# Performance work log

Hardware: AMD Instinct MI355X
Metric: run time of the kernel (lower is better)

## Reference

```python
import jax, jax.numpy as jnp
import numpy as np

D = 128           # volume / particle box size (pixels)
B = 8             # particles per batch
K = 125           # SO(3) grid poses (5x5x5 around each center Euler)
TOPK = 2          # keep_top_k_values
MAX_SHIFT_FRAC = 0.25  # main_config.projmatching.max_shift_fraction


def setup_inputs() -> dict:
    key = jax.random.key(0)
    k1, k2, k3, k4 = jax.random.split(key, 4)
    vol = jax.random.normal(k1, (D, D, D), dtype=jnp.float32)
    parts = jax.random.normal(k2, (B, D, D), dtype=jnp.float32)
    ctf = jax.random.uniform(k3, (B, D, D // 2 + 1), dtype=jnp.float32)
    euler_degs = jax.random.normal(k4, (K, 3), dtype=jnp.float32) * 8.0
    return {"vol": vol, "parts": parts, "ctf": ctf, "euler_degs": euler_degs}


def _rot_z(t):
    c, s = jnp.cos(t), jnp.sin(t)
    z, o = jnp.zeros_like(t), jnp.ones_like(t)
    return jnp.stack([jnp.stack([c, -s, z], -1),
                      jnp.stack([s, c, z], -1),
                      jnp.stack([z, z, o], -1)], -2)


def _rot_y(t):
    c, s = jnp.cos(t), jnp.sin(t)
    z, o = jnp.zeros_like(t), jnp.ones_like(t)
    return jnp.stack([jnp.stack([c, z, s], -1),
                      jnp.stack([z, o, z], -1),
                      jnp.stack([-s, z, c], -1)], -2)


def euler_zyz_to_matrix(degs):
    # RELION Euler convention ZYZ: R = Rz(a) @ Ry(b) @ Rz(c)
    rad = jnp.deg2rad(degs)
    return _rot_z(rad[..., 0]) @ _rot_y(rad[..., 1]) @ _rot_z(rad[..., 2])


def trilinear_sample(vol, zi, yi, xi):
    # vol: (Dz, Dy, W) complex64; coords: (K, h, w) float32 array indices
    Dz, Dy, W = vol.shape
    z0, y0, x0 = jnp.floor(zi), jnp.floor(yi), jnp.floor(xi)
    tz, ty, tx = zi - z0, yi - y0, xi - x0
    out = jnp.zeros(zi.shape, dtype=vol.dtype)
    for dz in (0, 1):
        wz = tz if dz else 1.0 - tz
        zc = z0 + dz
        vz = (zc >= 0) & (zc < Dz)
        zdx = jnp.clip(zc, 0, Dz - 1).astype(jnp.int32)
        for dy in (0, 1):
            wy = ty if dy else 1.0 - ty
            yc = y0 + dy
            vy = (yc >= 0) & (yc < Dy)
            ydx = jnp.clip(yc, 0, Dy - 1).astype(jnp.int32)
            for dx in (0, 1):
                wx = tx if dx else 1.0 - tx
                xc = x0 + dx
                vx = (xc >= 0) & (xc < W)
                xdx = jnp.clip(xc, 0, W - 1).astype(jnp.int32)
                w = jnp.where(vz & vy & vx, wz * wy * wx, 0.0)
                out = out + w * vol[zdx, ydx, xdx]
    return out


def project_fourier(vol_rfft, rotmats):
    # extract_central_slices_rfft: pose-dependent gather+trilinear interp of a
    # central slice from the fftshifted 3D rfft volume. Output: (K, D, D//2+1).
    d = D
    w = d // 2 + 1
    y = jnp.arange(d, dtype=jnp.float32) - d // 2   # fftshifted full-dim freqs (pixel units)
    x = jnp.arange(w, dtype=jnp.float32)            # rfft (non-negative) freqs
    yy, xx = jnp.meshgrid(y, x, indexing='ij')      # (d, w)
    coords = jnp.stack([xx, yy, jnp.zeros_like(yy)], -1)       # xyz, (d, w, 3), z = 0 plane
    rot = jnp.einsum('kij,hwj->khwi', rotmats, coords)          # (K, d, w, 3) rotated xyz
    conj_mask = rot[..., 0] < 0                                  # Hermitian symmetry: flip to x>=0 half
    rot = jnp.where(conj_mask[..., None], -rot, rot)
    xi = rot[..., 0]
    yi = rot[..., 1] + d // 2
    zi = rot[..., 2] + d // 2
    samples = trilinear_sample(vol_rfft, zi, yi, xi)
    samples = jnp.where(conj_mask, jnp.conj(samples), samples)
    r2 = xx ** 2 + yy ** 2                                       # zero beyond Nyquist radius
    samples = jnp.where(r2[None] > (d // 2) ** 2, 0.0, samples)
    return samples


def reference(vol, parts, ctf, euler_degs):
    # compute_dft: rfft volume, fftshift non-rfft dims
    vol_rfft = jnp.fft.fftshift(jnp.fft.rfftn(vol), axes=(0, 1))
    parts_rfft = jnp.fft.fftshift(jnp.fft.rfft2(parts), axes=(-2,))  # (B, D, W)
    rotmats = euler_zyz_to_matrix(euler_degs)                        # (K, 3, 3)
    projs = project_fourier(vol_rfft, rotmats)                       # (K, D, W)
    projs = ctf[:, None] * projs[None]                               # _apply_ctfF: (B, K, D, W)
    # correlate_dft_2d: cross-correlation via iFFT of parts * conj(projs)
    prod = parts_rfft[:, None] * jnp.conj(projs)
    prod = jnp.fft.ifftshift(prod, axes=(-2,))
    corr = jnp.fft.irfft2(prod, s=(D, D))                            # (B, K, D, D)
    corr = jnp.fft.fftshift(corr, axes=(-2, -1))                     # zero shift at center
    # _extract_ccor_max: restrict to |shift| <= max_shift_fraction*D, take top-k peaks
    center = D // 2
    max_shift = int(MAX_SHIFT_FRAC * D)
    idx = jnp.arange(D) - center
    win = (jnp.abs(idx)[:, None] <= max_shift) & (jnp.abs(idx)[None, :] <= max_shift)
    masked = jnp.where(win, corr, -jnp.inf)
    flat = masked.reshape(B, K, D * D)
    vals, top_idx = jax.lax.top_k(flat, TOPK)                        # (B, K, TOPK)
    shifts = jnp.stack([top_idx // D - center, top_idx % D - center], -1)  # (B, K, TOPK, 2) yx
    return vals, shifts
```

## Files before the change

### kernel.cpp

```cpp
#include <hip/hip_runtime.h>
#include <math.h>

#define D 128
#define W 65
#define NK 125
#define NB 8
#define SLAB (D*W)
#define TWO_PI 6.28318530717958647692f
#define R2C 0.70710678118654752440f
#define C8C 0.92387953251128675613f
#define S8C 0.38268343236508977173f


__device__ __forceinline__ bool better(float va, int ia, float vb, int ib) {
    return (va > vb) || (va == vb && ia < ib);
}
__device__ __forceinline__ float2 cmul(float2 a, float2 b) {
    return make_float2(a.x*b.x - a.y*b.y, a.x*b.y + a.y*b.x);
}
__device__ __forceinline__ void cmac(float2& acc, float2 a, float2 b) {
    acc.x = fmaf(a.x, b.x, fmaf(-a.y, b.y, acc.x));
    acc.y = fmaf(a.x, b.y, fmaf( a.y, b.x, acc.y));
}
__device__ __forceinline__ float2 cadd(float2 a, float2 b){ return make_float2(a.x+b.x, a.y+b.y); }
__device__ __forceinline__ float2 csub(float2 a, float2 b){ return make_float2(a.x-b.x, a.y-b.y); }

__device__ __forceinline__ void fft8_fwd(const float2* x, float2* a) {
    float2 e0 = x[0], o0 = x[1], e1 = x[2], o1 = x[3];
    float2 e2 = x[4], o2 = x[5], e3 = x[6], o3 = x[7];
    float2 t0 = cadd(e0, e2), t1 = csub(e0, e2);
    float2 t2 = cadd(e1, e3), t3 = csub(e1, e3);
    float2 E0 = cadd(t0, t2), E2 = csub(t0, t2);
    float2 E1 = make_float2(t1.x + t3.y, t1.y - t3.x);
    float2 E3 = make_float2(t1.x - t3.y, t1.y + t3.x);
    float2 u0 = cadd(o0, o2), u1 = csub(o0, o2);
    float2 u2 = cadd(o1, o3), u3 = csub(o1, o3);
    float2 O0 = cadd(u0, u2), O2 = csub(u0, u2);
    float2 O1 = make_float2(u1.x + u3.y, u1.y - u3.x);
    float2 O3 = make_float2(u1.x - u3.y, u1.y + u3.x);
    float2 w1 = make_float2(R2C*(O1.x + O1.y), R2C*(O1.y - O1.x));
    float2 w2 = make_float2(O2.y, -O2.x);
    float2 w3 = make_float2(R2C*(O3.y - O3.x), -R2C*(O3.x + O3.y));
    a[0] = cadd(E0, O0); a[4] = csub(E0, O0);
    a[1] = cadd(E1, w1); a[5] = csub(E1, w1);
    a[2] = cadd(E2, w2); a[6] = csub(E2, w2);
    a[3] = cadd(E3, w3); a[7] = csub(E3, w3);
}

__device__ __forceinline__ void ifft8_store(float2* __restrict__ Ab, const float2* p,
                                            int l, int m0) {
    float2 e0 = p[0], o0 = p[1], e1 = p[2], o1 = p[3];
    float2 e2 = p[4], o2 = p[5], e3 = p[6], o3 = p[7];
    float2 t0 = cadd(e0, e2), t1 = csub(e0, e2);
    float2 t2 = cadd(e1, e3), t3 = csub(e1, e3);
    float2 E0 = cadd(t0, t2), E2 = csub(t0, t2);
    float2 E1 = make_float2(t1.x - t3.y, t1.y + t3.x);
    float2 E3 = make_float2(t1.x + t3.y, t1.y - t3.x);
    float2 u0 = cadd(o0, o2), u1 = csub(o0, o2);
    float2 u2 = cadd(o1, o3), u3 = csub(o1, o3);
    float2 O0 = cadd(u0, u2), O2 = csub(u0, u2);
    float2 O1 = make_float2(u1.x - u3.y, u1.y + u3.x);
    float2 O3 = make_float2(u1.x + u3.y, u1.y - u3.x);
    float2 w1o = make_float2(R2C*(O1.x - O1.y), R2C*(O1.x + O1.y));
    float2 w2o = make_float2(-O2.y, O2.x);
    float2 w3o = make_float2(R2C*(-O3.x - O3.y), R2C*(O3.x - O3.y));
    float2* A = Ab + l * 144 + m0;
    A[0*18] = cadd(E0, O0);
    A[4*18] = csub(E0, O0);
    A[1*18] = cadd(E1, w1o);
    A[5*18] = csub(E1, w1o);
    A[2*18] = cadd(E2, w2o);
    A[6*18] = csub(E2, w2o);
    A[3*18] = cadd(E3, w3o);
    A[7*18] = csub(E3, w3o);
}


template<int MODE>
__device__ __forceinline__ void fft128v2(const float* __restrict__ inf,
                                         const float2* __restrict__ inc,
                                         float2* __restrict__ out,
                                         int l0, int nlines,
                                         float2* __restrict__ Fl,
                                         float2* __restrict__ twf) {
    int tid = threadIdx.x;
    int line, t;
    if (MODE == 0) { t = tid & 7; line = tid >> 3; }
    else           { line = tid & 31; t = tid >> 5; }
    int l = l0 + line;
    bool live = (l < nlines);

    if (tid < 128) {
        float s, c;
        sincosf(-TWO_PI * (float)tid / 128.0f, &s, &c);
        twf[tid] = make_float2(c, s);
    }

    int base = 0, stride = 1;
    if (MODE == 1 || MODE == 3) { base = (l / W) * SLAB + (l % W); stride = W; }
    else if (MODE == 2) { base = l; stride = SLAB; }

    float2 xe[8], xo[8];
    if (live) {
        if (MODE == 0) {
            const float* r = inf + (size_t)l * D;
            #pragma unroll
            for (int j = 0; j < 8; ++j) {
                xe[j] = make_float2(r[t + 16*j], 0.f);
                xo[j] = make_float2(r[t + 8 + 16*j], 0.f);
            }
        } else {
            #pragma unroll
            for (int j = 0; j < 8; ++j) {
                xe[j] = inc[base + (t + 16*j) * stride];
                xo[j] = inc[base + (t + 8 + 16*j) * stride];
            }
        }
    } else {
        #pragma unroll
        for (int j = 0; j < 8; ++j) { xe[j] = make_float2(0,0); xo[j] = make_float2(0,0); }
    }
    float2 E[8], O[8];
    fft8_fwd(xe, E);
    fft8_fwd(xo, O);
    {
        const float2 w16[8] = {
            { 1.f, 0.f }, { C8C, -S8C }, { R2C, -R2C }, { S8C, -C8C },
            { 0.f, -1.f }, { -S8C, -C8C }, { -R2C, -R2C }, { -C8C, -S8C }
        };
        float2* Fp = Fl + line * 137 + t * 17;
        #pragma unroll
        for (int kk = 0; kk < 8; ++kk) {
            float2 wo = cmul(w16[kk], O[kk]);
            Fp[kk]     = cadd(E[kk], wo);
            Fp[kk + 8] = csub(E[kk], wo);
        }
    }
    __syncthreads();
    if (live) {
        const float2* Fr = Fl + line * 137;
        #pragma unroll
        for (int s = 0; s < 16; ++s) {
            int slot = t + 8 * s;
            if (MODE == 0 && slot > 64) break;
            int k = (MODE == 0) ? slot : (slot ^ 64);
            int kk = k & 15;
            float2 acc = make_float2(0.f, 0.f);
            #pragma unroll
            for (int tt = 0; tt < 8; ++tt) {
                cmac(acc, Fr[tt * 17 + kk], twf[(tt * k) & 127]);
            }
            if (MODE == 0)      out[(size_t)l * W + slot] = acc;
            else if (MODE == 3) out[(size_t)l * D + slot] = acc;
            else                out[base + slot * stride] = acc;
        }
    }
}


__global__ __launch_bounds__(256) void k1_kernel(const float* __restrict__ vol,
                                                 const float* __restrict__ parts,
                                                 const float* __restrict__ ctf,
                                                 const float* __restrict__ euler,
                                                 float2* __restrict__ bufA,
                                                 float2* __restrict__ pT1,
                                                 float* __restrict__ CT,
                                                 float* __restrict__ rot) {
    __shared__ float2 Fl[32 * 137];
    __shared__ float2 twf[128];
    int bid = blockIdx.x;
    int tid = threadIdx.x;
    if (bid < 512) {
        fft128v2<0>(vol, nullptr, bufA, bid * 32, D*D, Fl, twf);
    } else if (bid < 544) {
        fft128v2<0>(parts, nullptr, pT1, (bid - 512) * 32, NB*D, Fl, twf);
    } else if (bid == 544) {
        int k = tid;
        if (k < NK) {
            const float d2r = 0.017453292519943295f;
            float a = euler[k*3+0]*d2r, b = euler[k*3+1]*d2r, c = euler[k*3+2]*d2r;
            float sa, ca, sb, cb, sc, cc;
            sincosf(a, &sa, &ca); sincosf(b, &sb, &cb); sincosf(c, &sc, &cc);
            rot[k*9+0] =  ca*cb*cc - sa*sc;
            rot[k*9+1] = -ca*cb*sc - sa*cc;
            rot[k*9+2] =  ca*sb;
            rot[k*9+3] =  sa*cb*cc + ca*sc;
            rot[k*9+4] = -sa*cb*sc + ca*cc;
            rot[k*9+5] =  sa*sb;
            rot[k*9+6] = -sb*cc;
            rot[k*9+7] =  sb*sc;
            rot[k*9+8] =  cb;
        }
    } else {
        int i = (bid - 545) * 256 + tid;
        if (i < NB * W * D) {
            int m = i & (D-1);
            int t2 = i >> 7;
            int x = t2 % W;
            int b = t2 / W;
            CT[i] = ctf[b * SLAB + m * W + x];
        }
    }
}

__global__ __launch_bounds__(256) void k2_kernel(const float2* __restrict__ bufA,
                                                 float2* __restrict__ bufB,
                                                 const float2* __restrict__ pT1,
                                                 float2* __restrict__ QT) {
    __shared__ float2 Fl[32 * 137];
    __shared__ float2 twf[128];
    int bid = blockIdx.x;
    if (bid < 260) fft128v2<1>(nullptr, bufA, bufB, bid * 32, D*W, Fl, twf);
    else           fft128v2<3>(nullptr, pT1, QT, (bid - 260) * 32, NB*W, Fl, twf);
}

__global__ __launch_bounds__(256) void k3_kernel(const float2* __restrict__ bufB,
                                                 float2* __restrict__ bufA) {
    __shared__ float2 Fl[32 * 137];
    __shared__ float2 twf[128];
    fft128v2<2>(nullptr, bufB, bufA, blockIdx.x * 32, SLAB, Fl, twf);
}


__global__ void proj_kernel(const float2* __restrict__ vol, const float* __restrict__ rot,
                            float2* __restrict__ projT) {
    int idx = blockIdx.x * blockDim.x + threadIdx.x;
    if (idx >= NK * D * W) return;
    int h = idx & (D-1);
    int t2 = idx >> 7;
    int w = t2 % W;
    int k = t2 / W;
    float x = (float)w;
    float y = (float)(h - 64);
    const float* R = rot + k*9;
    float rx = R[0]*x + R[1]*y;
    float ry = R[3]*x + R[4]*y;
    float rz = R[6]*x + R[7]*y;
    bool neg = rx < 0.0f;
    if (neg) { rx = -rx; ry = -ry; rz = -rz; }
    float xi = rx;
    float yi = ry + 64.0f;
    float zi = rz + 64.0f;
    float z0 = floorf(zi), y0 = floorf(yi), x0 = floorf(xi);
    float tz = zi - z0, ty = yi - y0, tx = xi - x0;
    int z0i = (int)z0, y0i = (int)y0, x0i = (int)x0;
    float ar = 0.f, ai = 0.f;
    for (int dz = 0; dz < 2; ++dz) {
        float wz = dz ? tz : 1.0f - tz;
        int zc = z0i + dz;
        bool vz = (zc >= 0) && (zc < D);
        int zx = min(max(zc, 0), D-1);
        for (int dy = 0; dy < 2; ++dy) {
            float wy = dy ? ty : 1.0f - ty;
            int yc = y0i + dy;
            bool vy = (yc >= 0) && (yc < D);
            int yx = min(max(yc, 0), D-1);
            for (int dx = 0; dx < 2; ++dx) {
                float wx = dx ? tx : 1.0f - tx;
                int xc = x0i + dx;
                bool vx = (xc >= 0) && (xc < W);
                int xx = min(max(xc, 0), W-1);
                float wt = (vz && vy && vx) ? wz*wy*wx : 0.0f;
                float2 v = vol[zx * SLAB + yx * W + xx];
                ar = fmaf(wt, v.x, ar);
                ai = fmaf(wt, v.y, ai);
            }
        }
    }
    if (neg) ai = -ai;
    int yy = h - 64;
    if (w*w + yy*yy > 4096) { ar = 0.f; ai = 0.f; }
    projT[idx] = make_float2(ar, ai);
}


__global__ __launch_bounds__(256, 2) void corr_kernel(const float2* __restrict__ QT,
                                                      const float*  __restrict__ CT,
                                                      const float2* __restrict__ PJT,
                                                      float* __restrict__ outv) {
    __shared__ float2 tw[128];
    __shared__ float2 Ab[17*144];
    __shared__ float2 BC[32*67];
    __shared__ float  Ny[65];
    __shared__ float  redv[8];
    __shared__ int    redi[8];

    int g = blockIdx.x;
    int logical = (g & 7) * 125 + (g >> 3);
    int k = logical >> 3;
    int b = logical & 7;
    int tid = threadIdx.x;
    const float inv_d = 1.0f / 128.0f;

    if (tid < 128) {
        float s, c;
        sincosf(TWO_PI * (float)tid / 128.0f, &s, &c);
        tw[tid] = make_float2(c, s);
    }

    const float2* Qb = QT + b * (W * D);
    const float*  Cb = CT + b * (W * D);
    const float2* Jk = PJT + k * (W * D);

    int lane = tid & 63;
    int wv = tid >> 6;
    int sv = lane & 7;
    int vp = (96 + lane) & 127;
    float acc[16];
    #pragma unroll
    for (int j = 0; j < 16; ++j) acc[j] = 0.0f;
    float accR = 0.0f;
    int ur = 0, vr = 0;
    if (tid < 129) { if (tid < 65) { ur = 64; vr = tid; } else { ur = tid - 65; vr = 64; } }

    __syncthreads();

    float2 wvp = tw[vp];
    float2 tq = make_float2(1.0f, 0.0f);

    int l1 = tid >> 4, m01 = tid & 15;
    float2 Qv[8]; float Cv[8]; float2 Jv[8];

    for (int cg = 0; cg < 4; ++cg) {
        if (cg == 0) {
            for (int i = tid; i < 17 * 16; i += 256) {
                int l = i >> 4, m0 = i & 15;
                int x = (l < 16) ? ((l >> 2) + 16 * (l & 3)) : 64;
                const float2* Qx = Qb + x * 128 + m0;
                const float*  Cx = Cb + x * 128 + m0;
                const float2* Jx = Jk + x * 128 + m0;
                float2 p[8];
                #pragma unroll
                for (int j = 0; j < 8; ++j) {
                    float2 qv = Qx[16*j];
                    float  cf = Cx[16*j];
                    float2 pj = Jx[16*j];
                    float sx = qv.x * cf, sy = qv.y * cf;
                    p[j] = make_float2(sx*pj.x + sy*pj.y, sy*pj.x - sx*pj.y);
                }
                ifft8_store(Ab, p, l, m0);
            }
        } else {
            float2 p[8];
            #pragma unroll
            for (int j = 0; j < 8; ++j) {
                float sx = Qv[j].x * Cv[j], sy = Qv[j].y * Cv[j];
                p[j] = make_float2(sx*Jv[j].x + sy*Jv[j].y, sy*Jv[j].x - sx*Jv[j].y);
            }
            ifft8_store(Ab, p, l1, m01);
        }
        __syncthreads();
        if (cg < 3) {
            int xn = 4*(cg+1) + (l1 >> 2) + 16 * (l1 & 3);
            const float2* Qx = Qb + xn * 128 + m01;
            const float*  Cx = Cb + xn * 128 + m01;
            const float2* Jx = Jk + xn * 128 + m01;
            #pragma unroll
            for (int j = 0; j < 8; ++j) {
                Qv[j] = Qx[16*j];
                Cv[j] = Cx[16*j];
                Jv[j] = Jx[16*j];
            }
        }
        {
            int lim = (cg == 0) ? 325 : 260;
            for (int i = tid; i < lim; i += 256) {
                if (i < 260) {
                    int q = i / 65;
                    int u2 = i - q * 65;
                    int r = u2 & 7, up = (96 + u2) & 127;
                    float2 wup = tw[up];
                    float2 wup2 = cmul(wup, wup);
                    const float4* A0 = (const float4*)(Ab + (4*q+0)*144 + r*18);
                    const float4* A1 = (const float4*)(Ab + (4*q+1)*144 + r*18);
                    const float4* A2 = (const float4*)(Ab + (4*q+2)*144 + r*18);
                    const float4* A3 = (const float4*)(Ab + (4*q+3)*144 + r*18);
                    float2 g0{0,0}, g1{0,0}, g2{0,0}, g3{0,0};
                    float2 tA = make_float2(1.0f, 0.0f);
                    #pragma unroll
                    for (int h = 0; h < 8; ++h) {
                        float2 tB = cmul(tA, wup);
                        float4 a;
                        a = A0[h]; cmac(g0, make_float2(a.x,a.y), tA); cmac(g0, make_float2(a.z,a.w), tB);
                        a = A1[h]; cmac(g1, make_float2(a.x,a.y), tA); cmac(g1, make_float2(a.z,a.w), tB);
                        a = A2[h]; cmac(g2, make_float2(a.x,a.y), tA); cmac(g2, make_float2(a.z,a.w), tB);
                        a = A3[h]; cmac(g3, make_float2(a.x,a.y), tA); cmac(g3, make_float2(a.z,a.w), tB);
                        tA = cmul(tA, wup2);
                    }
                    float sg = (u2 & 1) ? -inv_d : inv_d;
                    g0.x *= sg; g0.y *= sg; g1.x *= sg; g1.y *= sg;
                    g2.x *= sg; g2.y *= sg; g3.x *= sg; g3.y *= sg;
                    if (cg == 0 && q == 0) { g0.x *= 0.5f; g0.y *= 0.5f; }
                    float2 h0 = g0, h1 = g1, h2 = g2, h3 = g3;
                    const float sc = 2.0f * inv_d;
                    float2 p1 = make_float2(R2C*(h1.x - h1.y), R2C*(h1.x + h1.y));
                    float2 q1 = make_float2(R2C*(-h1.x - h1.y), R2C*(h1.x - h1.y));
                    float2 i1 = make_float2(-h1.y, h1.x);
                    float2 i2 = make_float2(-h2.y, h2.x);
                    float2 n2 = make_float2( h2.y, -h2.x);
                    float2 p3 = make_float2(R2C*(h3.x - h3.y), R2C*(h3.x + h3.y));
                    float2 q3 = make_float2(R2C*(-h3.x - h3.y), R2C*(h3.x - h3.y));
                    float2 i3 = make_float2(-h3.y, h3.x);
                    float2 a02 = cadd(h0, h2), s02 = csub(h0, h2);
                    float2 s0 = cadd(a02, cadd(h1, h3));
                    float2 s4 = csub(a02, cadd(h1, h3));
                    float2 s2 = cadd(s02, csub(i1, i3));
                    float2 s6 = csub(s02, csub(i1, i3));
                    float2 b0i = cadd(h0, i2);
                    float2 b0n = cadd(h0, n2);
                    float2 s1 = cadd(b0i, cadd(p1, q3));
                    float2 s5 = csub(b0i, cadd(p1, q3));
                    float2 s3 = cadd(b0n, cadd(q1, p3));
                    float2 s7 = csub(b0n, cadd(q1, p3));
                    float2* Bp = BC + q * (8*67) + u2;
                    Bp[0*67] = make_float2(s0.x*sc, s0.y*sc);
                    Bp[1*67] = make_float2(s1.x*sc, s1.y*sc);
                    Bp[2*67] = make_float2(s2.x*sc, s2.y*sc);
                    Bp[3*67] = make_float2(s3.x*sc, s3.y*sc);
                    Bp[4*67] = make_float2(s4.x*sc, s4.y*sc);
                    Bp[5*67] = make_float2(s5.x*sc, s5.y*sc);
                    Bp[6*67] = make_float2(s6.x*sc, s6.y*sc);
                    Bp[7*67] = make_float2(s7.x*sc, s7.y*sc);
                } else {
                    int u2 = i - 260;
                    int r = u2 & 7, up = (96 + u2) & 127;
                    float2 wup = tw[up];
                    float2 wup2 = cmul(wup, wup);
                    const float4* A = (const float4*)(Ab + 16*144 + r*18);
                    float re = 0.0f;
                    float2 tA = make_float2(1.0f, 0.0f);
                    #pragma unroll
                    for (int h = 0; h < 8; ++h) {
                        float2 tB = cmul(tA, wup);
                        float4 a = A[h];
                        re = fmaf(a.x, tA.x, fmaf(-a.y, tA.y, re));
                        re = fmaf(a.z, tB.x, fmaf(-a.w, tB.y, re));
                        tA = cmul(tA, wup2);
                    }
                    Ny[u2] = ((u2 & 1) ? -inv_d : inv_d) * re;
                }
            }
        }
        __syncthreads();
        {
            #pragma unroll
            for (int q = 0; q < 4; ++q) {
                const float2* Bq = BC + (q * 8 + sv) * 67 + wv * 16;
                float tx = tq.x, ty = tq.y;
                #pragma unroll
                for (int j = 0; j < 16; ++j) {
                    float2 bv = Bq[j];
                    acc[j] = fmaf(bv.x, tx, fmaf(-bv.y, ty, acc[j]));
                }
                tq = cmul(tq, wvp);
            }
            if (cg == 0) {
                float sgn = (lane & 1) ? -inv_d : inv_d;
                #pragma unroll
                for (int j = 0; j < 16; ++j) acc[j] = fmaf(sgn, Ny[wv * 16 + j], acc[j]);
            }
            if (tid < 129) {
                int sr = vr & 7, vpr = (96 + vr) & 127;
                float a = accR;
                #pragma unroll
                for (int q = 0; q < 4; ++q) {
                    float2 t = tw[((4*cg + q) * vpr) & 127];
                    float2 bv = BC[(q * 8 + sr) * 67 + ur];
                    a = fmaf(bv.x, t.x, fmaf(-bv.y, t.y, a));
                }
                if (cg == 0) a += (vr & 1) ? -inv_d * Ny[ur] : inv_d * Ny[ur];
                accR = a;
            }
        }
        __syncthreads();
    }

    float v1 = -INFINITY, v2 = -INFINITY;
    int i1 = 0x7fffffff, i2 = 0x7fffffff;
    #pragma unroll
    for (int j = 0; j < 16; ++j) {
        float val = acc[j];
        int uu = wv * 16 + j;
        int fl = (32 + uu) * D + (32 + lane);
        if (better(val, fl, v1, i1)) { v2 = v1; i2 = i1; v1 = val; i1 = fl; }
        else if (better(val, fl, v2, i2)) { v2 = val; i2 = fl; }
    }
    if (tid < 129) {
        int fl = (32 + ur) * D + (32 + vr);
        if (better(accR, fl, v1, i1)) { v2 = v1; i2 = i1; v1 = accR; i1 = fl; }
        else if (better(accR, fl, v2, i2)) { v2 = accR; i2 = fl; }
    }
    for (int off = 32; off > 0; off >>= 1) {
        float b1 = __shfl_down(v1, off); int j1 = __shfl_down(i1, off);
        float b2 = __shfl_down(v2, off); int j2 = __shfl_down(i2, off);
        if (better(b1, j1, v1, i1)) {
            float nv2; int ni2;
            if (better(v1, i1, b2, j2)) { nv2 = v1; ni2 = i1; } else { nv2 = b2; ni2 = j2; }
            v1 = b1; i1 = j1; v2 = nv2; i2 = ni2;
        } else {
            if (better(b1, j1, v2, i2)) { v2 = b1; i2 = j1; }
        }
    }
    int wave = tid >> 6;
    if ((tid & 63) == 0) {
        redv[wave*2]   = v1; redi[wave*2]   = i1;
        redv[wave*2+1] = v2; redi[wave*2+1] = i2;
    }
    __syncthreads();
    if (tid == 0) {
        float r1 = -INFINITY, r2 = -INFINITY;
        int q1 = 0x7fffffff, q2 = 0x7fffffff;
        for (int i = 0; i < 8; ++i) {
            float val = redv[i]; int fl = redi[i];
            if (better(val, fl, r1, q1)) { r2 = r1; q2 = q1; r1 = val; q1 = fl; }
            else if (better(val, fl, r2, q2)) { r2 = val; q2 = fl; }
        }
        int base = (b * NK + k) * 2;
        outv[base]     = r1;
        outv[base + 1] = r2;
        float* os = outv + NB*NK*2;
        os[(base    )*2 + 0] = (float)(q1 / D - 64);
        os[(base    )*2 + 1] = (float)(q1 % D - 64);
        os[(base + 1)*2 + 0] = (float)(q2 / D - 64);
        os[(base + 1)*2 + 1] = (float)(q2 % D - 64);
    }
}


extern "C" void kernel_launch(void* const* d_in, const int* in_sizes, int n_in,
                              void* d_out, int out_size, void* d_ws, size_t ws_size,
                              hipStream_t stream) {
    const float* vol   = (const float*)d_in[0];
    const float* parts = (const float*)d_in[1];
    const float* ctf   = (const float*)d_in[2];
    const float* euler = (const float*)d_in[3];
    float* out = (float*)d_out;

    const int VOLC = D * SLAB;
    float2* bufA   = (float2*)d_ws;
    float2* bufB   = bufA + VOLC;
    float2* pT1    = bufB + VOLC;
    float2* QT     = pT1 + NB * SLAB;
    float2* PJT    = QT + NB * W * D;
    float*  CT     = (float*)(PJT + NK * W * D);
    float*  rot    = CT + NB * W * D;

    k1_kernel<<<805, 256, 0, stream>>>(vol, parts, ctf, euler, bufA, pT1, CT, rot);
    k2_kernel<<<277, 256, 0, stream>>>(bufA, bufB, pT1, QT);
    k3_kernel<<<260, 256, 0, stream>>>(bufB, bufA);
    proj_kernel<<<(NK*D*W + 255) / 256, 256, 0, stream>>>(bufA, rot, PJT);
    corr_kernel<<<NB * NK, 256, 0, stream>>>(QT, CT, PJT, out);
}
```

Before: 91.95 us.

## Prefold CTF into particle spectrum and replace direct DFT with radix-16 FFT stage

The CTF multiply moves out of the per-(batch,pose) correlation kernel and into the particle column FFT (new MODE 4), so the correlation kernel loads one pre-scaled spectrum instead of a spectrum plus a CTF array. Inside the correlation kernel, the 16-point direct DFT over line groups (an 8-tap twiddle-recurrence dot product per output) becomes a twiddle multiply followed by a second radix-8/radix-2 butterfly stage writing into a new shared buffer G. The later stage then reads precomputed G entries instead of recomputing sums. This cuts ALU work and CTF memory traffic, at the cost of more shared memory (AbBC plus G) and an extra barrier per iteration.

Measured after the change: 83.23 us. 1.1x faster.

```diff
diff --git a/kernel.cpp b/kernel.cpp
--- a/kernel.cpp
+++ b/kernel.cpp
@@ -10,6 +10,8 @@
 #define R2C 0.70710678118654752440f
 #define C8C 0.92387953251128675613f
 #define S8C 0.38268343236508977173f
+#define ARS 146
+#define GRS 131
 
 
 __device__ __forceinline__ bool better(float va, int ia, float vb, int ib) {
@@ -47,10 +49,9 @@
     a[3] = cadd(E3, w3); a[7] = csub(E3, w3);
 }
 
-__device__ __forceinline__ void ifft8_store(float2* __restrict__ Ab, const float2* p,
-                                            int l, int m0) {
-    float2 e0 = p[0], o0 = p[1], e1 = p[2], o1 = p[3];
-    float2 e2 = p[4], o2 = p[5], e3 = p[6], o3 = p[7];
+__device__ __forceinline__ void ifft8_reg(const float2* x, float2* a) {
+    float2 e0 = x[0], o0 = x[1], e1 = x[2], o1 = x[3];
+    float2 e2 = x[4], o2 = x[5], e3 = x[6], o3 = x[7];
     float2 t0 = cadd(e0, e2), t1 = csub(e0, e2);
     float2 t2 = cadd(e1, e3), t3 = csub(e1, e3);
     float2 E0 = cadd(t0, t2), E2 = csub(t0, t2);
@@ -64,15 +65,10 @@
     float2 w1o = make_float2(R2C*(O1.x - O1.y), R2C*(O1.x + O1.y));
     float2 w2o = make_float2(-O2.y, O2.x);
     float2 w3o = make_float2(R2C*(-O3.x - O3.y), R2C*(O3.x - O3.y));
-    float2* A = Ab + l * 144 + m0;
-    A[0*18] = cadd(E0, O0);
-    A[4*18] = csub(E0, O0);
-    A[1*18] = cadd(E1, w1o);
-    A[5*18] = csub(E1, w1o);
-    A[2*18] = cadd(E2, w2o);
-    A[6*18] = csub(E2, w2o);
-    A[3*18] = cadd(E3, w3o);
-    A[7*18] = csub(E3, w3o);
+    a[0] = cadd(E0, O0); a[4] = csub(E0, O0);
+    a[1] = cadd(E1, w1o); a[5] = csub(E1, w1o);
+    a[2] = cadd(E2, w2o); a[6] = csub(E2, w2o);
+    a[3] = cadd(E3, w3o); a[7] = csub(E3, w3o);
 }
 
 
@@ -80,6 +76,7 @@
 __device__ __forceinline__ void fft128v2(const float* __restrict__ inf,
                                          const float2* __restrict__ inc,
                                          float2* __restrict__ out,
+                                         const float* __restrict__ ct,
                                          int l0, int nlines,
                                          float2* __restrict__ Fl,
                                          float2* __restrict__ twf) {
@@ -97,7 +94,7 @@
     }
 
     int base = 0, stride = 1;
-    if (MODE == 1 || MODE == 3) { base = (l / W) * SLAB + (l % W); stride = W; }
+    if (MODE == 1 || MODE == 3 || MODE == 4) { base = (l / W) * SLAB + (l % W); stride = W; }
     else if (MODE == 2) { base = l; stride = SLAB; }
 
     float2 xe[8], xo[8];
@@ -152,6 +149,10 @@
             }
             if (MODE == 0)      out[(size_t)l * W + slot] = acc;
             else if (MODE == 3) out[(size_t)l * D + slot] = acc;
+            else if (MODE == 4) {
+                float cf = ct[(size_t)l * D + slot];
+                out[(size_t)l * D + slot] = make_float2(acc.x * cf, acc.y * cf);
+            }
             else                out[base + slot * stride] = acc;
         }
     }
@@ -171,9 +172,9 @@
     int bid = blockIdx.x;
     int tid = threadIdx.x;
     if (bid < 512) {
-        fft128v2<0>(vol, nullptr, bufA, bid * 32, D*D, Fl, twf);
+        fft128v2<0>(vol, nullptr, bufA, nullptr, bid * 32, D*D, Fl, twf);
     } else if (bid < 544) {
-        fft128v2<0>(parts, nullptr, pT1, (bid - 512) * 32, NB*D, Fl, twf);
+        fft128v2<0>(parts, nullptr, pT1, nullptr, (bid - 512) * 32, NB*D, Fl, twf);
     } else if (bid == 544) {
         int k = tid;
         if (k < NK) {
@@ -206,19 +207,20 @@
 __global__ __launch_bounds__(256) void k2_kernel(const float2* __restrict__ bufA,
                                                  float2* __restrict__ bufB,
                                                  const float2* __restrict__ pT1,
-                                                 float2* __restrict__ QT) {
+                                                 float2* __restrict__ ST,
+                                                 const float* __restrict__ CT) {
     __shared__ float2 Fl[32 * 137];
     __shared__ float2 twf[128];
     int bid = blockIdx.x;
-    if (bid < 260) fft128v2<1>(nullptr, bufA, bufB, bid * 32, D*W, Fl, twf);
-    else           fft128v2<3>(nullptr, pT1, QT, (bid - 260) * 32, NB*W, Fl, twf);
+    if (bid < 260) fft128v2<1>(nullptr, bufA, bufB, nullptr, bid * 32, D*W, Fl, twf);
+    else           fft128v2<4>(nullptr, pT1, ST, CT, (bid - 260) * 32, NB*W, Fl, twf);
 }
 
 __global__ __launch_bounds__(256) void k3_kernel(const float2* __restrict__ bufB,
                                                  float2* __restrict__ bufA) {
     __shared__ float2 Fl[32 * 137];
     __shared__ float2 twf[128];
-    fft128v2<2>(nullptr, bufB, bufA, blockIdx.x * 32, SLAB, Fl, twf);
+    fft128v2<2>(nullptr, bufB, bufA, nullptr, blockIdx.x * 32, SLAB, Fl, twf);
 }
 
 
@@ -274,13 +276,12 @@
 }
 
 
-__global__ __launch_bounds__(256, 2) void corr_kernel(const float2* __restrict__ QT,
-                                                      const float*  __restrict__ CT,
+__global__ __launch_bounds__(256, 2) void corr_kernel(const float2* __restrict__ ST,
                                                       const float2* __restrict__ PJT,
                                                       float* __restrict__ outv) {
     __shared__ float2 tw[128];
-    __shared__ float2 Ab[17*144];
-    __shared__ float2 BC[32*67];
+    __shared__ float2 AbBC[17*ARS];
+    __shared__ float2 G[17*GRS];
     __shared__ float  Ny[65];
     __shared__ float  redv[8];
     __shared__ int    redi[8];
@@ -298,8 +299,7 @@
         tw[tid] = make_float2(c, s);
     }
 
-    const float2* Qb = QT + b * (W * D);
-    const float*  Cb = CT + b * (W * D);
+    const float2* Sb = ST + b * (W * D);
     const float2* Jk = PJT + k * (W * D);
 
     int lane = tid & 63;
@@ -319,79 +319,102 @@
     float2 tq = make_float2(1.0f, 0.0f);
 
     int l1 = tid >> 4, m01 = tid & 15;
-    float2 Qv[8]; float Cv[8]; float2 Jv[8];
+    float2 Sv[8], Jv[8];
 
     for (int cg = 0; cg < 4; ++cg) {
         if (cg == 0) {
             for (int i = tid; i < 17 * 16; i += 256) {
                 int l = i >> 4, m0 = i & 15;
                 int x = (l < 16) ? ((l >> 2) + 16 * (l & 3)) : 64;
-                const float2* Qx = Qb + x * 128 + m0;
-                const float*  Cx = Cb + x * 128 + m0;
+                const float2* Sx = Sb + x * 128 + m0;
                 const float2* Jx = Jk + x * 128 + m0;
                 float2 p[8];
                 #pragma unroll
                 for (int j = 0; j < 8; ++j) {
-                    float2 qv = Qx[16*j];
-                    float  cf = Cx[16*j];
+                    float2 s = Sx[16*j];
                     float2 pj = Jx[16*j];
-                    float sx = qv.x * cf, sy = qv.y * cf;
-                    p[j] = make_float2(sx*pj.x + sy*pj.y, sy*pj.x - sx*pj.y);
+                    p[j] = make_float2(s.x*pj.x + s.y*pj.y, s.y*pj.x - s.x*pj.y);
                 }
-                ifft8_store(Ab, p, l, m0);
+                float2 A[8];
+                ifft8_reg(p, A);
+                float2* dst = AbBC + l * ARS + m0;
+                dst[0] = A[0];
+                #pragma unroll
+                for (int r = 1; r < 8; ++r) dst[r*18] = cmul(A[r], tw[(r * m0) & 127]);
             }
         } else {
             float2 p[8];
             #pragma unroll
             for (int j = 0; j < 8; ++j) {
-                float sx = Qv[j].x * Cv[j], sy = Qv[j].y * Cv[j];
-                p[j] = make_float2(sx*Jv[j].x + sy*Jv[j].y, sy*Jv[j].x - sx*Jv[j].y);
-            }
-            ifft8_store(Ab, p, l1, m01);
+                p[j] = make_float2(Sv[j].x*Jv[j].x + Sv[j].y*Jv[j].y,
+                                   Sv[j].y*Jv[j].x - Sv[j].x*Jv[j].y);
+            }
+            float2 A[8];
+            ifft8_reg(p, A);
+            float2* dst = AbBC + l1 * ARS + m01;
+            dst[0] = A[0];
+            #pragma unroll
+            for (int r = 1; r < 8; ++r) dst[r*18] = cmul(A[r], tw[(r * m01) & 127]);
         }
         __syncthreads();
+        {
+            int lim2 = (cg == 0) ? 136 : 128;
+            for (int i = tid; i < lim2; i += 256) {
+                int l, r;
+                if (i < 128) { l = i & 15; r = i >> 4; }
+                else         { l = 16; r = i - 128; }
+                const float4* Ar = (const float4*)(AbBC + l * ARS + r * 18);
+                float2 xe[8], xo[8];
+                #pragma unroll
+                for (int j = 0; j < 8; ++j) {
+                    float4 a = Ar[j];
+                    xe[j] = make_float2(a.x, a.y);
+                    xo[j] = make_float2(a.z, a.w);
+                }
+                float2 E[8], O[8];
+                ifft8_reg(xe, E);
+                ifft8_reg(xo, O);
+                const float2 w16p[8] = {
+                    { 1.f, 0.f }, { C8C, S8C }, { R2C, R2C }, { S8C, C8C },
+                    { 0.f, 1.f }, { -S8C, C8C }, { -R2C, R2C }, { -C8C, S8C }
+                };
+                float2* Gl = G + l * GRS + r;
+                #pragma unroll
+                for (int t = 0; t < 8; ++t) {
+                    float2 wo = cmul(w16p[t], O[t]);
+                    Gl[8*t]      = cadd(E[t], wo);
+                    Gl[8*t + 64] = csub(E[t], wo);
+                }
+            }
+        }
         if (cg < 3) {
             int xn = 4*(cg+1) + (l1 >> 2) + 16 * (l1 & 3);
-            const float2* Qx = Qb + xn * 128 + m01;
-            const float*  Cx = Cb + xn * 128 + m01;
+            const float2* Sx = Sb + xn * 128 + m01;
             const float2* Jx = Jk + xn * 128 + m01;
             #pragma unroll
             for (int j = 0; j < 8; ++j) {
-                Qv[j] = Qx[16*j];
-                Cv[j] = Cx[16*j];
+                Sv[j] = Sx[16*j];
                 Jv[j] = Jx[16*j];
             }
         }
+        __syncthreads();
         {
+            float2* BC = AbBC;
             int lim = (cg == 0) ? 325 : 260;
             for (int i = tid; i < lim; i += 256) {
                 if (i < 260) {
                     int q = i / 65;
                     int u2 = i - q * 65;
-                    int r = u2 & 7, up = (96 + u2) & 127;
-                    float2 wup = tw[up];
-                    float2 wup2 = cmul(wup, wup);
-                    const float4* A0 = (const float4*)(Ab + (4*q+0)*144 + r*18);
-                    const float4* A1 = (const float4*)(Ab + (4*q+1)*144 + r*18);
-                    const float4* A2 = (const float4*)(Ab + (4*q+2)*144 + r*18);
-                    const float4* A3 = (const float4*)(Ab + (4*q+3)*144 + r*18);
-                    float2 g0{0,0}, g1{0,0}, g2{0,0}, g3{0,0};
-                    float2 tA = make_float2(1.0f, 0.0f);
-                    #pragma unroll
-                    for (int h = 0; h < 8; ++h) {
-                        float2 tB = cmul(tA, wup);
-                        float4 a;
-                        a = A0[h]; cmac(g0, make_float2(a.x,a.y), tA); cmac(g0, make_float2(a.z,a.w), tB);
-                        a = A1[h]; cmac(g1, make_float2(a.x,a.y), tA); cmac(g1, make_float2(a.z,a.w), tB);
-                        a = A2[h]; cmac(g2, make_float2(a.x,a.y), tA); cmac(g2, make_float2(a.z,a.w), tB);
-                        a = A3[h]; cmac(g3, make_float2(a.x,a.y), tA); cmac(g3, make_float2(a.z,a.w), tB);
-                        tA = cmul(tA, wup2);
-                    }
+                    int up = (96 + u2) & 127;
                     float sg = (u2 & 1) ? -inv_d : inv_d;
-                    g0.x *= sg; g0.y *= sg; g1.x *= sg; g1.y *= sg;
-                    g2.x *= sg; g2.y *= sg; g3.x *= sg; g3.y *= sg;
-                    if (cg == 0 && q == 0) { g0.x *= 0.5f; g0.y *= 0.5f; }
-                    float2 h0 = g0, h1 = g1, h2 = g2, h3 = g3;
+                    const float2* Gq = G + up;
+                    float2 h0 = Gq[(4*q+0)*GRS];
+                    float2 h1 = Gq[(4*q+1)*GRS];
+                    float2 h2 = Gq[(4*q+2)*GRS];
+                    float2 h3 = Gq[(4*q+3)*GRS];
+                    h0.x *= sg; h0.y *= sg; h1.x *= sg; h1.y *= sg;
+                    h2.x *= sg; h2.y *= sg; h3.x *= sg; h3.y *= sg;
+                    if (cg == 0 && q == 0) { h0.x *= 0.5f; h0.y *= 0.5f; }
                     const float sc = 2.0f * inv_d;
                     float2 p1 = make_float2(R2C*(h1.x - h1.y), R2C*(h1.x + h1.y));
                     float2 q1 = make_float2(R2C*(-h1.x - h1.y), R2C*(h1.x - h1.y));
@@ -423,26 +446,14 @@
                     Bp[7*67] = make_float2(s7.x*sc, s7.y*sc);
                 } else {
                     int u2 = i - 260;
-                    int r = u2 & 7, up = (96 + u2) & 127;
-                    float2 wup = tw[up];
-                    float2 wup2 = cmul(wup, wup);
-                    const float4* A = (const float4*)(Ab + 16*144 + r*18);
-                    float re = 0.0f;
-                    float2 tA = make_float2(1.0f, 0.0f);
-                    #pragma unroll
-                    for (int h = 0; h < 8; ++h) {
-                        float2 tB = cmul(tA, wup);
-                        float4 a = A[h];
-                        re = fmaf(a.x, tA.x, fmaf(-a.y, tA.y, re));
-                        re = fmaf(a.z, tB.x, fmaf(-a.w, tB.y, re));
-                        tA = cmul(tA, wup2);
-                    }
-                    Ny[u2] = ((u2 & 1) ? -inv_d : inv_d) * re;
+                    int up = (96 + u2) & 127;
+                    Ny[u2] = ((u2 & 1) ? -inv_d : inv_d) * G[16*GRS + up].x;
                 }
             }
         }
         __syncthreads();
         {
+            const float2* BC = AbBC;
             #pragma unroll
             for (int q = 0; q < 4; ++q) {
                 const float2* Bq = BC + (q * 8 + sv) * 67 + wv * 16;
@@ -465,7 +476,7 @@
                 #pragma unroll
                 for (int q = 0; q < 4; ++q) {
                     float2 t = tw[((4*cg + q) * vpr) & 127];
-                    float2 bv = BC[(q * 8 + sr) * 67 + ur];
+                    float2 bv = AbBC[(q * 8 + sr) * 67 + ur];
                     a = fmaf(bv.x, t.x, fmaf(-bv.y, t.y, a));
                 }
                 if (cg == 0) a += (vr & 1) ? -inv_d * Ny[ur] : inv_d * Ny[ur];
@@ -540,14 +551,14 @@
     float2* bufA   = (float2*)d_ws;
     float2* bufB   = bufA + VOLC;
     float2* pT1    = bufB + VOLC;
-    float2* QT     = pT1 + NB * SLAB;
-    float2* PJT    = QT + NB * W * D;
+    float2* ST     = pT1 + NB * SLAB;
+    float2* PJT    = ST + NB * W * D;
     float*  CT     = (float*)(PJT + NK * W * D);
     float*  rot    = CT + NB * W * D;
 
     k1_kernel<<<805, 256, 0, stream>>>(vol, parts, ctf, euler, bufA, pT1, CT, rot);
-    k2_kernel<<<277, 256, 0, stream>>>(bufA, bufB, pT1, QT);
+    k2_kernel<<<277, 256, 0, stream>>>(bufA, bufB, pT1, ST, CT);
     k3_kernel<<<260, 256, 0, stream>>>(bufB, bufA);
     proj_kernel<<<(NK*D*W + 255) / 256, 256, 0, stream>>>(bufA, rot, PJT);
-    corr_kernel<<<NB * NK, 256, 0, stream>>>(QT, CT, PJT, out);
-}
+    corr_kernel<<<NB * NK, 256, 0, stream>>>(ST, PJT, out);
+}
```
